# Kernel optimization log

Measured on AMD Instinct MI355X. Metric: run time of the kernel, lower is better.

Reference implementation:

```python
import jax, jax.numpy as jnp
import numpy as np

NLAT, NLON = 361, 720
LMAX = NLAT               # equiangular grid: lmax = nlat
MMAX = NLON // 2 + 1      # mmax = nlon//2 + 1
B, C = 1, 128


def _precompute_legpoly(mmax, lmax, t, csphase=True):
    """Associated Legendre vandermonde P_l^m(cos t), orthonormal, inverse=True
    (norm factor 1 for 'ortho'). Shape [mmax, lmax, nlat]. Setup-time numpy only."""
    x = np.cos(t)
    nmax = max(mmax, lmax)
    vdm = np.zeros((nmax, nmax, len(x)))
    vdm[0, 0] = np.sqrt(1.0 / (4.0 * np.pi))
    for l in range(1, nmax):
        vdm[l - 1, l] = np.sqrt(2 * l + 1) * x * vdm[l - 1, l - 1]
        vdm[l, l] = np.sqrt((2 * l + 1) * (1 + x) * (1 - x) / (2 * l)) * vdm[l - 1, l - 1]
    for l in range(2, nmax):
        for m in range(l - 1):
            a = np.sqrt((2 * l - 1) / (l - m) * (2 * l + 1) / (l + m))
            b = np.sqrt((l + m - 1) / (l - m) * (2 * l + 1) / (2 * l - 3) * (l - m - 1) / (l + m))
            vdm[m, l] = a * x * vdm[m, l - 1] - b * vdm[m, l - 2]
    vdm = vdm[:mmax, :lmax]
    if csphase:
        vdm[1::2] *= -1.0  # Condon-Shortley phase on odd m
    return vdm


def setup_inputs() -> dict:
    key = jax.random.key(0)
    # spherical harmonic coefficients as real view: [B, C, lmax, mmax, 2]
    x_real = jax.random.normal(key, (B, C, LMAX, MMAX, 2), dtype=jnp.float32)
    # equiangular (Clenshaw-Curtiss) colatitudes, t = flip(arccos(cos(pi*j/(n-1))))
    t = np.pi * np.arange(NLAT) / (NLAT - 1)
    pct = jnp.asarray(_precompute_legpoly(MMAX, LMAX, t), dtype=jnp.float32)  # [mmax, lmax, nlat]
    return {"x_real": x_real, "pct": pct}


def reference(x_real, pct):
    # single-device case: comm sizes == 1, all distributed transposes are identity
    # and nlatpad == nlonpad == 0.
    # per-m triangular Legendre contraction over l (torch einsum '...lmr,mlk->...kmr')
    xs = jnp.einsum('bclmr,mlk->bckmr', x_real, pct)        # [B, C, nlat, mmax, 2]
    xc = jax.lax.complex(xs[..., 0], xs[..., 1])            # [B, C, nlat, mmax]
    # inverse real FFT along longitude, norm='forward' (no 1/n scaling on inverse)
    out = jnp.fft.irfft(xc, n=NLON, axis=-1, norm='forward')  # [B, C, nlat, nlon]
    return out.astype(x_real.dtype)
```

## Files before the change

### kernel.cpp

```cpp
#include <hip/hip_runtime.h>
#include <cstddef>

#define CC   128
#define LDIM 361
#define MDIM 361
#define KDIM 361
#define NLON 720
#define LP   384
#define MRP  736
#define NP   768
#define CK   (CC*KDIM)
#define CR   (2*CC)

typedef __attribute__((ext_vector_type(8))) short short8;
typedef __attribute__((ext_vector_type(4))) float floatx4;

__device__ __forceinline__ unsigned short f2bf(float f) {
    union { float f; unsigned u; } v; v.f = f;
    unsigned u = v.u;
    u += 0x7fffu + ((u >> 16) & 1u);
    return (unsigned short)(u >> 16);
}

__device__ __forceinline__ void async_copy16(const void* g, void* l) {
    __builtin_amdgcn_global_load_lds(
        (const __attribute__((address_space(1))) void*)g,
        (__attribute__((address_space(3))) void*)l, 16, 0, 0);
}

__global__ void sht_gen_T(unsigned short* __restrict__ Tp) {
    int idx = blockIdx.x * 256 + threadIdx.x;
    if (idx >= NP * MRP) return;
    int n = idx / MRP, mr = idx - n * MRP;
    float v = 0.f;
    if (n < NLON && mr < 2 * MDIM) {
        int m = mr >> 1, im = mr & 1;
        if (m == 0)            v = im ? 0.f : 1.f;
        else if (m == MDIM-1)  v = im ? 0.f : ((n & 1) ? -1.f : 1.f);
        else {
            int ph = (m * n) % NLON;
            float ang = (float)ph * (float)(3.14159265358979323846 / 360.0);
            v = im ? (-2.f * sinf(ang)) : (2.f * cosf(ang));
        }
    }
    Tp[idx] = f2bf(v);
}

__global__ __launch_bounds__(256)
void sht_prep_x(const float* __restrict__ x, unsigned short* __restrict__ xA) {
    __shared__ float2 tile[64][33];
    const int mt = blockIdx.x;
    const int lt = blockIdx.y;
    const int c  = blockIdx.z;
    const int t  = threadIdx.x;

    #pragma unroll
    for (int u = 0; u < 8; ++u) {
        int p  = t + 256 * u;
        int li = p >> 5, mi = p & 31;
        int l = lt * 64 + li, m = mt * 32 + mi;
        float2 v = make_float2(0.f, 0.f);
        if (l < LDIM && m < MDIM)
            v = *(const float2*)(x + ((size_t)(c * LDIM + l) * MDIM + m) * 2);
        tile[li][mi] = v;
    }
    __syncthreads();

    #pragma unroll
    for (int u = 0; u < 2; ++u) {
        int s  = t + 256 * u;
        int mi = s >> 4, rr = (s >> 3) & 1, lo = (s & 7) * 8;
        int m = mt * 32 + mi;
        if (m >= MDIM) continue;
        short8 h;
        #pragma unroll
        for (int e = 0; e < 8; ++e) {
            float2 p = tile[lo + e][mi];
            h[e] = (short)f2bf(rr ? p.y : p.x);
        }
        *(short8*)(xA + ((size_t)m * CR + 2 * c + rr) * LP + lt * 64 + lo) = h;
    }
}

__global__ __launch_bounds__(256)
void sht_stageA(const float* __restrict__ pct, const unsigned short* __restrict__ xA,
                unsigned short* __restrict__ xs) {
    __shared__ unsigned short As[128 * 32];
    __shared__ unsigned short Bs[32 * 130];

    const int m   = blockIdx.y;
    const int ct  = blockIdx.x & 1;
    const int kt  = blockIdx.x >> 1;
    const int c0  = ct * 128;
    const int n0  = kt * 128;
    const int t   = threadIdx.x;
    const int w   = t >> 6, L = t & 63;
    const int wr  = w & 1, wc = w >> 1;
    const int lane15 = L & 15, quad = L >> 4;
    const int bl = t >> 3, bkq = t & 7;

    const unsigned short* xAm = xA + (size_t)m * CR * LP;
    const float* pctm = pct + (size_t)m * LDIM * KDIM;

    floatx4 acc[4][4] = {};

    for (int kb = 0; kb < LP; kb += 32) {
        #pragma unroll
        for (int i = 0; i < 2; ++i) {
            int s = w * 128 + i * 64 + L;
            int cr = s >> 2, lq = s & 3;
            async_copy16(xAm + (size_t)(c0 + cr) * LP + kb + lq * 8,
                         As + (size_t)(w * 128 + i * 64) * 8);
        }
        {
            int l = kb + bl;
            bool lok = (l < LDIM);
            const float* prow = pctm + (size_t)l * KDIM;
            #pragma unroll
            for (int u = 0; u < 4; ++u) {
                int kc = n0 + u * 32 + bkq * 4;
                float f0 = (lok && kc + 0 < KDIM) ? prow[kc + 0] : 0.f;
                float f1 = (lok && kc + 1 < KDIM) ? prow[kc + 1] : 0.f;
                float f2 = (lok && kc + 2 < KDIM) ? prow[kc + 2] : 0.f;
                float f3 = (lok && kc + 3 < KDIM) ? prow[kc + 3] : 0.f;
                unsigned* bp = (unsigned*)&Bs[bl * 130 + u * 32 + bkq * 4];
                bp[0] = (unsigned)f2bf(f0) | ((unsigned)f2bf(f1) << 16);
                bp[1] = (unsigned)f2bf(f2) | ((unsigned)f2bf(f3) << 16);
            }
        }
        __syncthreads();

        short8 af[4];
        #pragma unroll
        for (int i = 0; i < 4; ++i) {
            int row = wr * 64 + i * 16 + lane15;
            af[i] = *(const short8*)&As[(row * 4 + quad) * 8];
        }
        #pragma unroll
        for (int jf = 0; jf < 4; ++jf) {
            int col = wc * 64 + jf * 16 + lane15;
            short8 bf;
            #pragma unroll
            for (int j = 0; j < 8; ++j)
                bf[j] = (short)Bs[(quad * 8 + j) * 130 + col];
            #pragma unroll
            for (int i = 0; i < 4; ++i)
                acc[i][jf] = __builtin_amdgcn_mfma_f32_16x16x32_bf16(af[i], bf, acc[i][jf], 0, 0, 0);
        }
        __syncthreads();
    }

    #pragma unroll
    for (int i = 0; i < 4; ++i) {
        #pragma unroll
        for (int jf = 0; jf < 4; ++jf) {
            int k = n0 + wc * 64 + jf * 16 + lane15;
            if (k >= KDIM) continue;
            #pragma unroll
            for (int eh = 0; eh < 2; ++eh) {
                int cr = c0 + wr * 64 + i * 16 + quad * 4 + eh * 2;
                int c  = cr >> 1;
                unsigned pack = (unsigned)f2bf(acc[i][jf][eh * 2]) |
                                ((unsigned)f2bf(acc[i][jf][eh * 2 + 1]) << 16);
                *(unsigned*)(xs + (size_t)(c * KDIM + k) * MRP + 2 * m) = pack;
            }
        }
    }
}

__global__ __launch_bounds__(256)
void sht_stageB(const unsigned short* __restrict__ xs, const unsigned short* __restrict__ Tp,
                float* __restrict__ out) {
    __shared__ unsigned short As[128 * 32];
    __shared__ unsigned short Bs[128 * 32];

    const int nt  = blockIdx.x;
    const int ckt = blockIdx.y;
    const int ck0 = ckt * 128, n0 = nt * 128;
    const int t   = threadIdx.x;
    const int w   = t >> 6, L = t & 63;
    const int wr  = w & 1, wc = w >> 1;
    const int lane15 = L & 15, quad = L >> 4;

    floatx4 acc[4][4] = {};

    for (int kb = 0; kb < MRP; kb += 32) {
        #pragma unroll
        for (int i = 0; i < 2; ++i) {
            int s = w * 128 + i * 64 + L;
            int rr = s >> 2, mq = s & 3;
            async_copy16(xs + (size_t)(ck0 + rr) * MRP + kb + mq * 8,
                         As + (size_t)(w * 128 + i * 64) * 8);
            async_copy16(Tp + (size_t)(n0 + rr) * MRP + kb + mq * 8,
                         Bs + (size_t)(w * 128 + i * 64) * 8);
        }
        __syncthreads();

        short8 af[4], bfr[4];
        #pragma unroll
        for (int i = 0; i < 4; ++i)
            af[i] = *(const short8*)&As[((wr * 64 + i * 16 + lane15) * 4 + quad) * 8];
        #pragma unroll
        for (int jf = 0; jf < 4; ++jf)
            bfr[jf] = *(const short8*)&Bs[((wc * 64 + jf * 16 + lane15) * 4 + quad) * 8];
        #pragma unroll
        for (int i = 0; i < 4; ++i)
            #pragma unroll
            for (int jf = 0; jf < 4; ++jf)
                acc[i][jf] = __builtin_amdgcn_mfma_f32_16x16x32_bf16(af[i], bfr[jf], acc[i][jf], 0, 0, 0);
        __syncthreads();
    }

    #pragma unroll
    for (int i = 0; i < 4; ++i) {
        int ckr = ck0 + wr * 64 + i * 16 + quad * 4;
        #pragma unroll
        for (int jf = 0; jf < 4; ++jf) {
            int j = n0 + wc * 64 + jf * 16 + lane15;
            if (j >= NLON) continue;
            #pragma unroll
            for (int e = 0; e < 4; ++e)
                out[(size_t)(ckr + e) * NLON + j] = acc[i][jf][e];
        }
    }
}

extern "C" void kernel_launch(void* const* d_in, const int* in_sizes, int n_in,
                              void* d_out, int out_size, void* d_ws, size_t ws_size,
                              hipStream_t stream) {
    const float* x   = (const float*)d_in[0];
    const float* pct = (const float*)d_in[1];
    float* out = (float*)d_out;

    unsigned short* xs = (unsigned short*)d_ws;
    unsigned short* Tp = xs + (size_t)CK * MRP;
    unsigned short* xA = (unsigned short*)d_out;

    sht_gen_T<<<(NP * MRP + 255) / 256, 256, 0, stream>>>(Tp);
    sht_prep_x<<<dim3(12, 6, 128), 256, 0, stream>>>(x, xA);
    sht_stageA<<<dim3(6, MDIM), 256, 0, stream>>>(pct, xA, xs);
    sht_stageB<<<dim3(6, MDIM), 256, 0, stream>>>(xs, Tp, out);
}
```

Measured before the change: 725.9 us.

## Widen stage-A tiles to all channels and transpose output via separate kernel

Stage A now has each block cover all 256 channel-real rows, so pct is converted to bf16 once per k-tile instead of twice. The transposed B tile in shared memory is stored for vector reads. Results go to a contiguous m-major scratch buffer, and a new transpose kernel builds the ck-major layout stage B expects, replacing scattered 4-byte global stores. The cost is an extra kernel and an extra round trip of the intermediate through memory, with Tp reusing the scratch region after the transpose.

After: 803.6 us. 10.7% more time.

```diff
diff --git a/kernel.cpp b/kernel.cpp
--- a/kernel.cpp
+++ b/kernel.cpp
@@ -11,6 +11,7 @@
 #define NP   768
 #define CK   (CC*KDIM)
 #define CR   (2*CC)
+#define MR2  722
 
 typedef __attribute__((ext_vector_type(8))) short short8;
 typedef __attribute__((ext_vector_type(4))) float floatx4;
@@ -33,7 +34,7 @@
     if (idx >= NP * MRP) return;
     int n = idx / MRP, mr = idx - n * MRP;
     float v = 0.f;
-    if (n < NLON && mr < 2 * MDIM) {
+    if (n < NLON && mr < MR2) {
         int m = mr >> 1, im = mr & 1;
         if (m == 0)            v = im ? 0.f : 1.f;
         else if (m == MDIM-1)  v = im ? 0.f : ((n & 1) ? -1.f : 1.f);
@@ -84,65 +85,55 @@
 
 __global__ __launch_bounds__(256)
 void sht_stageA(const float* __restrict__ pct, const unsigned short* __restrict__ xA,
-                unsigned short* __restrict__ xs) {
-    __shared__ unsigned short As[128 * 32];
-    __shared__ unsigned short Bs[32 * 130];
-
-    const int m   = blockIdx.y;
-    const int ct  = blockIdx.x & 1;
-    const int kt  = blockIdx.x >> 1;
-    const int c0  = ct * 128;
-    const int n0  = kt * 128;
-    const int t   = threadIdx.x;
-    const int w   = t >> 6, L = t & 63;
-    const int wr  = w & 1, wc = w >> 1;
+                unsigned short* __restrict__ xs2) {
+    __shared__ unsigned short As[256 * 32];
+    __shared__ unsigned short Bs[128 * 40];
+
+    const int m  = blockIdx.y;
+    const int kt = blockIdx.x;
+    const int t  = threadIdx.x;
+    const int w  = t >> 6, L = t & 63;
     const int lane15 = L & 15, quad = L >> 4;
-    const int bl = t >> 3, bkq = t & 7;
+    const int tl = t >> 3;
+    const int tk = (t & 7) * 4;
 
     const unsigned short* xAm = xA + (size_t)m * CR * LP;
-    const float* pctm = pct + (size_t)m * LDIM * KDIM;
-
-    floatx4 acc[4][4] = {};
+    const float* pctm = pct + (size_t)m * LDIM * KDIM + (size_t)kt * 128;
+
+    floatx4 acc[4][8] = {};
 
     for (int kb = 0; kb < LP; kb += 32) {
         #pragma unroll
-        for (int i = 0; i < 2; ++i) {
-            int s = w * 128 + i * 64 + L;
+        for (int i = 0; i < 4; ++i) {
+            int s = (w * 4 + i) * 64 + L;
             int cr = s >> 2, lq = s & 3;
-            async_copy16(xAm + (size_t)(c0 + cr) * LP + kb + lq * 8,
-                         As + (size_t)(w * 128 + i * 64) * 8);
+            async_copy16(xAm + (size_t)cr * LP + kb + lq * 8,
+                         As + (size_t)(w * 4 + i) * 64 * 8);
         }
         {
-            int l = kb + bl;
+            int l = kb + tl;
             bool lok = (l < LDIM);
             const float* prow = pctm + (size_t)l * KDIM;
             #pragma unroll
             for (int u = 0; u < 4; ++u) {
-                int kc = n0 + u * 32 + bkq * 4;
-                float f0 = (lok && kc + 0 < KDIM) ? prow[kc + 0] : 0.f;
-                float f1 = (lok && kc + 1 < KDIM) ? prow[kc + 1] : 0.f;
-                float f2 = (lok && kc + 2 < KDIM) ? prow[kc + 2] : 0.f;
-                float f3 = (lok && kc + 3 < KDIM) ? prow[kc + 3] : 0.f;
-                unsigned* bp = (unsigned*)&Bs[bl * 130 + u * 32 + bkq * 4];
-                bp[0] = (unsigned)f2bf(f0) | ((unsigned)f2bf(f1) << 16);
-                bp[1] = (unsigned)f2bf(f2) | ((unsigned)f2bf(f3) << 16);
+                int kc = tk + u * 32;
+                int kg = kt * 128 + kc;
+                #pragma unroll
+                for (int j = 0; j < 4; ++j) {
+                    float f = (lok && (kg + j) < KDIM) ? prow[kc + j] : 0.f;
+                    Bs[(kc + j) * 40 + tl] = f2bf(f);
+                }
             }
         }
         __syncthreads();
 
         short8 af[4];
         #pragma unroll
-        for (int i = 0; i < 4; ++i) {
-            int row = wr * 64 + i * 16 + lane15;
-            af[i] = *(const short8*)&As[(row * 4 + quad) * 8];
-        }
-        #pragma unroll
-        for (int jf = 0; jf < 4; ++jf) {
-            int col = wc * 64 + jf * 16 + lane15;
-            short8 bf;
-            #pragma unroll
-            for (int j = 0; j < 8; ++j)
-                bf[j] = (short)Bs[(quad * 8 + j) * 130 + col];
+        for (int i = 0; i < 4; ++i)
+            af[i] = *(const short8*)&As[((w * 64 + i * 16 + lane15) * 4 + quad) * 8];
+        #pragma unroll
+        for (int jf = 0; jf < 8; ++jf) {
+            short8 bf = *(const short8*)&Bs[(jf * 16 + lane15) * 40 + quad * 8];
             #pragma unroll
             for (int i = 0; i < 4; ++i)
                 acc[i][jf] = __builtin_amdgcn_mfma_f32_16x16x32_bf16(af[i], bf, acc[i][jf], 0, 0, 0);
@@ -153,18 +144,48 @@
     #pragma unroll
     for (int i = 0; i < 4; ++i) {
         #pragma unroll
-        for (int jf = 0; jf < 4; ++jf) {
-            int k = n0 + wc * 64 + jf * 16 + lane15;
+        for (int jf = 0; jf < 8; ++jf) {
+            int k = kt * 128 + jf * 16 + lane15;
             if (k >= KDIM) continue;
             #pragma unroll
-            for (int eh = 0; eh < 2; ++eh) {
-                int cr = c0 + wr * 64 + i * 16 + quad * 4 + eh * 2;
-                int c  = cr >> 1;
-                unsigned pack = (unsigned)f2bf(acc[i][jf][eh * 2]) |
-                                ((unsigned)f2bf(acc[i][jf][eh * 2 + 1]) << 16);
-                *(unsigned*)(xs + (size_t)(c * KDIM + k) * MRP + 2 * m) = pack;
+            for (int e = 0; e < 4; ++e) {
+                int cr = w * 64 + i * 16 + quad * 4 + e;
+                int c = cr >> 1, r = cr & 1;
+                xs2[(size_t)(2 * m + r) * CK + (size_t)c * KDIM + k] = f2bf(acc[i][jf][e]);
             }
         }
+    }
+}
+
+__global__ __launch_bounds__(256)
+void sht_transpose(const unsigned short* __restrict__ xs2, unsigned short* __restrict__ xs) {
+    __shared__ unsigned short tile[64 * 72];
+    const int bk = blockIdx.x;
+    const int mt = blockIdx.y;
+    const int t  = threadIdx.x;
+
+    #pragma unroll
+    for (int u = 0; u < 2; ++u) {
+        int s = t + 256 * u;
+        int row = s >> 3, col8 = (s & 7) * 8;
+        int mr = mt * 64 + row;
+        short8 v = {};
+        if (mr < MR2)
+            v = *(const short8*)(xs2 + (size_t)mr * CK + bk * 64 + col8);
+        *(short8*)&tile[row * 72 + col8] = v;
+    }
+    __syncthreads();
+
+    #pragma unroll
+    for (int u = 0; u < 2; ++u) {
+        int s = t + 256 * u;
+        int cki = s >> 3, mo = (s & 7) * 8;
+        int mro = mt * 64 + mo;
+        if (mro >= MRP) continue;
+        short8 h;
+        #pragma unroll
+        for (int e = 0; e < 8; ++e) h[e] = tile[(mo + e) * 72 + cki];
+        *(short8*)(xs + (size_t)(bk * 64 + cki) * MRP + mro) = h;
     }
 }
 
@@ -232,12 +253,14 @@
     const float* pct = (const float*)d_in[1];
     float* out = (float*)d_out;
 
-    unsigned short* xs = (unsigned short*)d_ws;
-    unsigned short* Tp = xs + (size_t)CK * MRP;
-    unsigned short* xA = (unsigned short*)d_out;
-
+    unsigned short* xs  = (unsigned short*)d_ws;
+    unsigned short* xs2 = xs + (size_t)CK * MRP;
+    unsigned short* Tp  = xs2;
+    unsigned short* xA  = (unsigned short*)d_out;
+
+    sht_prep_x<<<dim3(12, 6, 128), 256, 0, stream>>>(x, xA);
+    sht_stageA<<<dim3(3, MDIM), 256, 0, stream>>>(pct, xA, xs2);
+    sht_transpose<<<dim3(722, 12), 256, 0, stream>>>(xs2, xs);
     sht_gen_T<<<(NP * MRP + 255) / 256, 256, 0, stream>>>(Tp);
-    sht_prep_x<<<dim3(12, 6, 128), 256, 0, stream>>>(x, xA);
-    sht_stageA<<<dim3(6, MDIM), 256, 0, stream>>>(pct, xA, xs);
     sht_stageB<<<dim3(6, MDIM), 256, 0, stream>>>(xs, Tp, out);
 }
```
